# Kernel optimization log

Hardware: AMD Instinct MI355X
Metric: run time of the kernel (lower is better)

## Reference

```python
import jax, jax.numpy as jnp
import numpy as np

BATCH, FIELD_DIM, EMBED_DIM = 16384, 2048, 64


def setup_inputs() -> dict:
    key = jax.random.key(0)
    k1, k2, k3 = jax.random.split(key, 3)
    x = jax.random.normal(k1, (BATCH, FIELD_DIM), dtype=jnp.float32)
    w = jax.random.normal(k2, (FIELD_DIM, 1), dtype=jnp.float32) * 0.02
    b = jnp.zeros((1,), dtype=jnp.float32)
    # FM factor matrix (xavier-normal-ish scale)
    v = jax.random.normal(k3, (FIELD_DIM, EMBED_DIM), dtype=jnp.float32) * (
        (2.0 / (FIELD_DIM + EMBED_DIM)) ** 0.5
    )
    return {"x": x, "w": w, "b": b, "v": v}


def reference(x, w, b, v):
    # First-order linear term: [B, 1]
    linear = x @ w + b
    # Second-order FM term, algebraic reformulation of the O(n^2) pairwise loop:
    # sum_{i<j} <v_i, v_j> x_i x_j = 0.5 * sum_k [(x @ v)_k^2 - (x^2 @ v^2)_k]
    xv = x @ v                       # [B, K]
    x2v2 = (x * x) @ (v * v)         # [B, K]
    second_order = 0.5 * jnp.sum(xv * xv - x2v2, axis=-1, keepdims=True)  # [B, 1]
    return jax.nn.sigmoid(linear + second_order)
```

## Files before the change

kernel.cpp:

```cpp
#include <hip/hip_runtime.h>
#include <stdint.h>

#define FD 2048

typedef short short8 __attribute__((ext_vector_type(8)));
typedef float f32x4 __attribute__((ext_vector_type(4)));
typedef unsigned short ushort_t;

__device__ __forceinline__ unsigned bf16_rne(float f) {
  unsigned u = __float_as_uint(f);
  return (u + 0x7FFFu + ((u >> 16) & 1u)) >> 16;
}

__global__ __launch_bounds__(256) void fm_prep(
    const float* __restrict__ v, ushort_t* __restrict__ hi,
    ushort_t* __restrict__ lo, float* __restrict__ s2t)
{
  int bid = blockIdx.x;
  if (bid < 512) {
    int t = bid * 256 + threadIdx.x;
    int j    = t & 7;
    int lane = (t >> 3) & 63;
    int c    = (t >> 9) & 3;
    int s    = t >> 11;
    int k    = s * 32 + ((lane >> 4) << 3) + j;
    int col  = (c << 4) + (lane & 15);
    float val = v[k * 64 + col];
    unsigned hb = bf16_rne(val);
    float hf = __uint_as_float(hb << 16);
    unsigned lb = bf16_rne(val - hf);
    hi[t] = (ushort_t)hb;
    lo[t] = (ushort_t)lb;
  } else {
    int k = (bid - 512) * 256 + threadIdx.x;
    const float4* row = (const float4*)(v + k * 64);
    float s = 0.f;
    #pragma unroll
    for (int i = 0; i < 16; ++i) {
      float4 q = row[i];
      s += q.x * q.x + q.y * q.y + q.z * q.z + q.w * q.w;
    }
    s2t[k] = s;
  }
}

__global__ __launch_bounds__(512) void fm_main(
    const float* __restrict__ x, const float* __restrict__ w,
    const float* __restrict__ bptr, const short8* __restrict__ vhi,
    const short8* __restrict__ vlo, const float* __restrict__ s2t,
    float* __restrict__ out)
{
  __shared__ float lds_xv[32][64];
  __shared__ float lds_lin[32];
  __shared__ float lds_q[32];

  const int tid = threadIdx.x;
  const int wv  = tid >> 6;
  const int l   = tid & 63;
  const int l15 = l & 15;
  const int lk  = l >> 4;
  const int R   = blockIdx.x << 5;
  const int kbase = wv << 8;

  {
    float* z = &lds_xv[0][0];
    #pragma unroll
    for (int i = tid; i < 32 * 64; i += 512) z[i] = 0.f;
    if (tid < 32) { lds_lin[tid] = 0.f; lds_q[tid] = 0.f; }
  }
  __syncthreads();

  const float* px0 = x + (size_t)(R + l15) * FD + kbase + (lk << 3);
  const float* px1 = px0 + (size_t)16 * FD;
  const float* pw  = w   + kbase + (lk << 3);
  const float* ps  = s2t + kbase + (lk << 3);

  f32x4 acc[2][4];
  #pragma unroll
  for (int t = 0; t < 2; ++t)
    #pragma unroll
    for (int c = 0; c < 4; ++c)
      acc[t][c] = (f32x4){0.f, 0.f, 0.f, 0.f};

  float lin0 = 0.f, lin1 = 0.f, q0 = 0.f, q1 = 0.f;

  #pragma unroll
  for (int st = 0; st < 8; ++st) {
    const int ko = st << 5;
    float4 a0 = *(const float4*)(px0 + ko);
    float4 a1 = *(const float4*)(px0 + ko + 4);
    float4 b0 = *(const float4*)(px1 + ko);
    float4 b1 = *(const float4*)(px1 + ko + 4);
    float4 w0 = *(const float4*)(pw + ko);
    float4 w1 = *(const float4*)(pw + ko + 4);
    float4 s0 = *(const float4*)(ps + ko);
    float4 s1 = *(const float4*)(ps + ko + 4);

    const int sg = (wv << 3) + st;
    short8 bh[4], bl[4];
    #pragma unroll
    for (int c = 0; c < 4; ++c) {
      bh[c] = vhi[(sg * 4 + c) * 64 + l];
      bl[c] = vlo[(sg * 4 + c) * 64 + l];
    }

    float fa[8] = {a0.x, a0.y, a0.z, a0.w, a1.x, a1.y, a1.z, a1.w};
    float fb[8] = {b0.x, b0.y, b0.z, b0.w, b1.x, b1.y, b1.z, b1.w};
    float fw[8] = {w0.x, w0.y, w0.z, w0.w, w1.x, w1.y, w1.z, w1.w};
    float fs[8] = {s0.x, s0.y, s0.z, s0.w, s1.x, s1.y, s1.z, s1.w};

    short8 ah0, al0, ah1, al1;
    #pragma unroll
    for (int j = 0; j < 8; ++j) {
      unsigned h0 = bf16_rne(fa[j]);
      ah0[j] = (short)h0;
      al0[j] = (short)bf16_rne(fa[j] - __uint_as_float(h0 << 16));
      lin0 = fmaf(fa[j], fw[j], lin0);
      q0   = fmaf(fa[j] * fa[j], fs[j], q0);
      unsigned h1 = bf16_rne(fb[j]);
      ah1[j] = (short)h1;
      al1[j] = (short)bf16_rne(fb[j] - __uint_as_float(h1 << 16));
      lin1 = fmaf(fb[j], fw[j], lin1);
      q1   = fmaf(fb[j] * fb[j], fs[j], q1);
    }

    #pragma unroll
    for (int c = 0; c < 4; ++c) {
      acc[0][c] = __builtin_amdgcn_mfma_f32_16x16x32_bf16(ah0, bh[c], acc[0][c], 0, 0, 0);
      acc[0][c] = __builtin_amdgcn_mfma_f32_16x16x32_bf16(al0, bh[c], acc[0][c], 0, 0, 0);
      acc[0][c] = __builtin_amdgcn_mfma_f32_16x16x32_bf16(ah0, bl[c], acc[0][c], 0, 0, 0);
      acc[1][c] = __builtin_amdgcn_mfma_f32_16x16x32_bf16(ah1, bh[c], acc[1][c], 0, 0, 0);
      acc[1][c] = __builtin_amdgcn_mfma_f32_16x16x32_bf16(al1, bh[c], acc[1][c], 0, 0, 0);
      acc[1][c] = __builtin_amdgcn_mfma_f32_16x16x32_bf16(ah1, bl[c], acc[1][c], 0, 0, 0);
    }
  }

  lin0 += __shfl_xor(lin0, 16, 64); lin0 += __shfl_xor(lin0, 32, 64);
  lin1 += __shfl_xor(lin1, 16, 64); lin1 += __shfl_xor(lin1, 32, 64);
  q0   += __shfl_xor(q0,   16, 64); q0   += __shfl_xor(q0,   32, 64);
  q1   += __shfl_xor(q1,   16, 64); q1   += __shfl_xor(q1,   32, 64);
  if (lk == 0) {
    atomicAdd(&lds_lin[l15],      lin0);
    atomicAdd(&lds_lin[16 + l15], lin1);
    atomicAdd(&lds_q[l15],        q0);
    atomicAdd(&lds_q[16 + l15],   q1);
  }

  #pragma unroll
  for (int t = 0; t < 2; ++t)
    #pragma unroll
    for (int c = 0; c < 4; ++c)
      #pragma unroll
      for (int j = 0; j < 4; ++j)
        atomicAdd(&lds_xv[t * 16 + lk * 4 + j][c * 16 + l15], acc[t][c][j]);

  __syncthreads();

  {
    const int row = tid >> 4;
    const int cg  = tid & 15;
    float4 s = *(const float4*)&lds_xv[row][cg << 2];
    float ss = s.x * s.x + s.y * s.y + s.z * s.z + s.w * s.w;
    ss += __shfl_xor(ss, 1, 64);
    ss += __shfl_xor(ss, 2, 64);
    ss += __shfl_xor(ss, 4, 64);
    ss += __shfl_xor(ss, 8, 64);
    if (cg == 0) {
      float z = lds_lin[row] + bptr[0] + 0.5f * (ss - lds_q[row]);
      out[R + row] = 1.f / (1.f + expf(-z));
    }
  }
}

extern "C" void kernel_launch(void* const* d_in, const int* in_sizes, int n_in,
                              void* d_out, int out_size, void* d_ws, size_t ws_size,
                              hipStream_t stream) {
  const float* x = (const float*)d_in[0];
  const float* w = (const float*)d_in[1];
  const float* b = (const float*)d_in[2];
  const float* v = (const float*)d_in[3];
  float* out = (float*)d_out;

  ushort_t* hi = (ushort_t*)d_ws;
  ushort_t* lo = hi + FD * 64;
  float*    s2 = (float*)((char*)d_ws + (size_t)FD * 64 * 2 * sizeof(ushort_t));

  fm_prep<<<520, 256, 0, stream>>>(v, hi, lo, s2);
  fm_main<<<512, 512, 0, stream>>>(x, w, b, (const short8*)hi, (const short8*)lo, s2, out);
}
```

Measured before the change: 256.1 us.

## Software-pipeline x loads and bf16 split conversion, stage w and s2 in LDS

Restructures the main loop so the next step's x tile is loaded and converted to hi/lo bf16 while the current step's MFMAs run, with the MFMAs reordered to group by A operand. The w and s2t vectors are staged once into LDS instead of being reloaded from global memory by every wave. Launch bounds now request 4 blocks per CU. The aim is to hide global-load latency in this memory-bound kernel. The cost is extra register pressure from holding the converted operands across iterations, plus 16 KB more LDS per block.

```diff
diff --git a/kernel.cpp b/kernel.cpp
--- a/kernel.cpp
+++ b/kernel.cpp
@@ -44,12 +44,35 @@
   }
 }
 
-__global__ __launch_bounds__(512) void fm_main(
+__device__ __forceinline__ void cvt_row(
+    const float4& A0, const float4& A1,
+    const float4& W0, const float4& W1,
+    const float4& S0, const float4& S1,
+    short8& H, short8& L, float& lin, float& q)
+{
+  float f[8]  = {A0.x, A0.y, A0.z, A0.w, A1.x, A1.y, A1.z, A1.w};
+  float fw[8] = {W0.x, W0.y, W0.z, W0.w, W1.x, W1.y, W1.z, W1.w};
+  float fs[8] = {S0.x, S0.y, S0.z, S0.w, S1.x, S1.y, S1.z, S1.w};
+  #pragma unroll
+  for (int j = 0; j < 8; ++j) {
+    unsigned h = bf16_rne(f[j]);
+    H[j] = (short)h;
+    L[j] = (short)bf16_rne(f[j] - __uint_as_float(h << 16));
+    lin = fmaf(f[j], fw[j], lin);
+    q   = fmaf(f[j] * f[j], fs[j], q);
+  }
+}
+
+#define MF(accv, a, b) accv = __builtin_amdgcn_mfma_f32_16x16x32_bf16(a, b, accv, 0, 0, 0)
+
+__global__ __launch_bounds__(512, 4) void fm_main(
     const float* __restrict__ x, const float* __restrict__ w,
     const float* __restrict__ bptr, const short8* __restrict__ vhi,
     const short8* __restrict__ vlo, const float* __restrict__ s2t,
     float* __restrict__ out)
 {
+  __shared__ float lds_w[FD];
+  __shared__ float lds_s[FD];
   __shared__ float lds_xv[32][64];
   __shared__ float lds_lin[32];
   __shared__ float lds_q[32];
@@ -67,13 +90,16 @@
     #pragma unroll
     for (int i = tid; i < 32 * 64; i += 512) z[i] = 0.f;
     if (tid < 32) { lds_lin[tid] = 0.f; lds_q[tid] = 0.f; }
+    *(float4*)&lds_w[tid << 2] = *(const float4*)(w + (tid << 2));
+    *(float4*)&lds_s[tid << 2] = *(const float4*)(s2t + (tid << 2));
   }
   __syncthreads();
 
   const float* px0 = x + (size_t)(R + l15) * FD + kbase + (lk << 3);
   const float* px1 = px0 + (size_t)16 * FD;
-  const float* pw  = w   + kbase + (lk << 3);
-  const float* ps  = s2t + kbase + (lk << 3);
+  const int wsoff = kbase + (lk << 3);
+  const short8* pb = vhi + (size_t)wv * 2048 + l;
+  const short8* pl = vlo + (size_t)wv * 2048 + l;
 
   f32x4 acc[2][4];
   #pragma unroll
@@ -84,54 +110,63 @@
 
   float lin0 = 0.f, lin1 = 0.f, q0 = 0.f, q1 = 0.f;
 
+  short8 cah0, cal0, cah1, cal1;
+  {
+    float4 a0 = *(const float4*)(px0);
+    float4 a1 = *(const float4*)(px0 + 4);
+    float4 b0 = *(const float4*)(px1);
+    float4 b1 = *(const float4*)(px1 + 4);
+    float4 wa = *(const float4*)&lds_w[wsoff];
+    float4 wb = *(const float4*)&lds_w[wsoff + 4];
+    float4 sa = *(const float4*)&lds_s[wsoff];
+    float4 sb = *(const float4*)&lds_s[wsoff + 4];
+    cvt_row(a0, a1, wa, wb, sa, sb, cah0, cal0, lin0, q0);
+    cvt_row(b0, b1, wa, wb, sa, sb, cah1, cal1, lin1, q1);
+  }
+
   #pragma unroll
   for (int st = 0; st < 8; ++st) {
-    const int ko = st << 5;
-    float4 a0 = *(const float4*)(px0 + ko);
-    float4 a1 = *(const float4*)(px0 + ko + 4);
-    float4 b0 = *(const float4*)(px1 + ko);
-    float4 b1 = *(const float4*)(px1 + ko + 4);
-    float4 w0 = *(const float4*)(pw + ko);
-    float4 w1 = *(const float4*)(pw + ko + 4);
-    float4 s0 = *(const float4*)(ps + ko);
-    float4 s1 = *(const float4*)(ps + ko + 4);
-
-    const int sg = (wv << 3) + st;
-    short8 bh[4], bl[4];
-    #pragma unroll
-    for (int c = 0; c < 4; ++c) {
-      bh[c] = vhi[(sg * 4 + c) * 64 + l];
-      bl[c] = vlo[(sg * 4 + c) * 64 + l];
-    }
-
-    float fa[8] = {a0.x, a0.y, a0.z, a0.w, a1.x, a1.y, a1.z, a1.w};
-    float fb[8] = {b0.x, b0.y, b0.z, b0.w, b1.x, b1.y, b1.z, b1.w};
-    float fw[8] = {w0.x, w0.y, w0.z, w0.w, w1.x, w1.y, w1.z, w1.w};
-    float fs[8] = {s0.x, s0.y, s0.z, s0.w, s1.x, s1.y, s1.z, s1.w};
-
-    short8 ah0, al0, ah1, al1;
-    #pragma unroll
-    for (int j = 0; j < 8; ++j) {
-      unsigned h0 = bf16_rne(fa[j]);
-      ah0[j] = (short)h0;
-      al0[j] = (short)bf16_rne(fa[j] - __uint_as_float(h0 << 16));
-      lin0 = fmaf(fa[j], fw[j], lin0);
-      q0   = fmaf(fa[j] * fa[j], fs[j], q0);
-      unsigned h1 = bf16_rne(fb[j]);
-      ah1[j] = (short)h1;
-      al1[j] = (short)bf16_rne(fb[j] - __uint_as_float(h1 << 16));
-      lin1 = fmaf(fb[j], fw[j], lin1);
-      q1   = fmaf(fb[j] * fb[j], fs[j], q1);
-    }
-
-    #pragma unroll
-    for (int c = 0; c < 4; ++c) {
-      acc[0][c] = __builtin_amdgcn_mfma_f32_16x16x32_bf16(ah0, bh[c], acc[0][c], 0, 0, 0);
-      acc[0][c] = __builtin_amdgcn_mfma_f32_16x16x32_bf16(al0, bh[c], acc[0][c], 0, 0, 0);
-      acc[0][c] = __builtin_amdgcn_mfma_f32_16x16x32_bf16(ah0, bl[c], acc[0][c], 0, 0, 0);
-      acc[1][c] = __builtin_amdgcn_mfma_f32_16x16x32_bf16(ah1, bh[c], acc[1][c], 0, 0, 0);
-      acc[1][c] = __builtin_amdgcn_mfma_f32_16x16x32_bf16(al1, bh[c], acc[1][c], 0, 0, 0);
-      acc[1][c] = __builtin_amdgcn_mfma_f32_16x16x32_bf16(ah1, bl[c], acc[1][c], 0, 0, 0);
+    float4 na0, na1, nb0, nb1;
+    if (st < 7) {
+      const int nko = (st + 1) << 5;
+      na0 = *(const float4*)(px0 + nko);
+      na1 = *(const float4*)(px0 + nko + 4);
+      nb0 = *(const float4*)(px1 + nko);
+      nb1 = *(const float4*)(px1 + nko + 4);
+    }
+
+    short8 bh0 = pb[st * 256 + 0];
+    short8 bh1 = pb[st * 256 + 64];
+    short8 bh2 = pb[st * 256 + 128];
+    short8 bh3 = pb[st * 256 + 192];
+
+    MF(acc[0][0], cah0, bh0); MF(acc[0][1], cah0, bh1);
+    MF(acc[0][2], cah0, bh2); MF(acc[0][3], cah0, bh3);
+    MF(acc[1][0], cah1, bh0); MF(acc[1][1], cah1, bh1);
+    MF(acc[1][2], cah1, bh2); MF(acc[1][3], cah1, bh3);
+    MF(acc[0][0], cal0, bh0); MF(acc[0][1], cal0, bh1);
+    MF(acc[0][2], cal0, bh2); MF(acc[0][3], cal0, bh3);
+    MF(acc[1][0], cal1, bh0); MF(acc[1][1], cal1, bh1);
+    MF(acc[1][2], cal1, bh2); MF(acc[1][3], cal1, bh3);
+
+    short8 bl0 = pl[st * 256 + 0];
+    short8 bl1 = pl[st * 256 + 64];
+    short8 bl2 = pl[st * 256 + 128];
+    short8 bl3 = pl[st * 256 + 192];
+
+    MF(acc[0][0], cah0, bl0); MF(acc[0][1], cah0, bl1);
+    MF(acc[0][2], cah0, bl2); MF(acc[0][3], cah0, bl3);
+    MF(acc[1][0], cah1, bl0); MF(acc[1][1], cah1, bl1);
+    MF(acc[1][2], cah1, bl2); MF(acc[1][3], cah1, bl3);
+
+    if (st < 7) {
+      const int nws = wsoff + ((st + 1) << 5);
+      float4 wa = *(const float4*)&lds_w[nws];
+      float4 wb = *(const float4*)&lds_w[nws + 4];
+      float4 sa = *(const float4*)&lds_s[nws];
+      float4 sb = *(const float4*)&lds_s[nws + 4];
+      cvt_row(na0, na1, wa, wb, sa, sb, cah0, cal0, lin0, q0);
+      cvt_row(nb0, nb1, wa, wb, sa, sb, cah1, cal1, lin1, q1);
     }
   }
 
```

Measured after the change: 246.0 us. 3.9% less time.

## Stage x tiles into swizzled double-buffered LDS via async global_load_lds

Applied to the files above, without the earlier changes.

Replaces the direct strided per-lane global loads of x with a loop over eight K-tiles. Each tile of 32 rows by 256 columns is copied asynchronously into a double-buffered, XOR-swizzled LDS buffer with global_load_lds, so the next tile's load overlaps the current tile's bf16 split and MFMA work. Work across waves is re-partitioned so all eight waves share each tile instead of each owning a contiguous 256-wide K slice. This adds 64KB of LDS per block plus a barrier per tile, which limits occupancy and adds synchronisation cost.

```diff
diff --git a/kernel.cpp b/kernel.cpp
--- a/kernel.cpp
+++ b/kernel.cpp
@@ -2,10 +2,13 @@
 #include <stdint.h>
 
 #define FD 2048
+#define BK 256
 
 typedef short short8 __attribute__((ext_vector_type(8)));
 typedef float f32x4 __attribute__((ext_vector_type(4)));
 typedef unsigned short ushort_t;
+typedef __attribute__((address_space(3))) char lds_char;
+typedef __attribute__((address_space(1))) const char glb_char;
 
 __device__ __forceinline__ unsigned bf16_rne(float f) {
   unsigned u = __float_as_uint(f);
@@ -44,23 +47,59 @@
   }
 }
 
-__global__ __launch_bounds__(512) void fm_main(
+__device__ __forceinline__ void cvt_row(
+    const f32x4& A0, const f32x4& A1,
+    const f32x4& W0v, const f32x4& W1v,
+    const f32x4& S0, const f32x4& S1,
+    short8& H, short8& L, float& lin, float& q)
+{
+  #pragma unroll
+  for (int j = 0; j < 8; ++j) {
+    float f  = (j < 4) ? A0[j & 3] : A1[j & 3];
+    float fw = (j < 4) ? W0v[j & 3] : W1v[j & 3];
+    float fs = (j < 4) ? S0[j & 3] : S1[j & 3];
+    unsigned h = bf16_rne(f);
+    H[j] = (short)h;
+    L[j] = (short)bf16_rne(f - __uint_as_float(h << 16));
+    lin = fmaf(f, fw, lin);
+    q   = fmaf(f * f, fs, q);
+  }
+}
+
+#define MF(accv, a, b) accv = __builtin_amdgcn_mfma_f32_16x16x32_bf16(a, b, accv, 0, 0, 0)
+
+__global__ __launch_bounds__(512, 4) void fm_main(
     const float* __restrict__ x, const float* __restrict__ w,
     const float* __restrict__ bptr, const short8* __restrict__ vhi,
     const short8* __restrict__ vlo, const float* __restrict__ s2t,
     float* __restrict__ out)
 {
+  __shared__ float xbuf[2][32][BK];
   __shared__ float lds_xv[32][64];
   __shared__ float lds_lin[32];
   __shared__ float lds_q[32];
 
   const int tid = threadIdx.x;
-  const int wv  = tid >> 6;
+  const int wid = tid >> 6;
   const int l   = tid & 63;
   const int l15 = l & 15;
   const int lk  = l >> 4;
+  const int l4  = l << 4;
   const int R   = blockIdx.x << 5;
-  const int kbase = wv << 8;
+
+  #define STAGE(t, b)                                                        \
+    {                                                                        \
+      _Pragma("unroll")                                                      \
+      for (int j = 0; j < 4; ++j) {                                          \
+        const int row = (wid << 2) + j;                                      \
+        const char* src = (const char*)x +                                   \
+            (((size_t)(R + row) << 11) + ((size_t)(t) << 8)) * 4 +           \
+            (size_t)(l4 ^ ((row & 7) << 4));                                 \
+        char* dst = (char*)&xbuf[b][row][0];                                 \
+        __builtin_amdgcn_global_load_lds((glb_char*)src, (lds_char*)dst,     \
+                                         16, 0, 0);                          \
+      }                                                                      \
+    }
 
   {
     float* z = &lds_xv[0][0];
@@ -68,12 +107,8 @@
     for (int i = tid; i < 32 * 64; i += 512) z[i] = 0.f;
     if (tid < 32) { lds_lin[tid] = 0.f; lds_q[tid] = 0.f; }
   }
+  STAGE(0, 0);
   __syncthreads();
-
-  const float* px0 = x + (size_t)(R + l15) * FD + kbase + (lk << 3);
-  const float* px1 = px0 + (size_t)16 * FD;
-  const float* pw  = w   + kbase + (lk << 3);
-  const float* ps  = s2t + kbase + (lk << 3);
 
   f32x4 acc[2][4];
   #pragma unroll
@@ -81,58 +116,58 @@
     #pragma unroll
     for (int c = 0; c < 4; ++c)
       acc[t][c] = (f32x4){0.f, 0.f, 0.f, 0.f};
-
   float lin0 = 0.f, lin1 = 0.f, q0 = 0.f, q1 = 0.f;
 
-  #pragma unroll
-  for (int st = 0; st < 8; ++st) {
-    const int ko = st << 5;
-    float4 a0 = *(const float4*)(px0 + ko);
-    float4 a1 = *(const float4*)(px0 + ko + 4);
-    float4 b0 = *(const float4*)(px1 + ko);
-    float4 b1 = *(const float4*)(px1 + ko + 4);
-    float4 w0 = *(const float4*)(pw + ko);
-    float4 w1 = *(const float4*)(pw + ko + 4);
-    float4 s0 = *(const float4*)(ps + ko);
-    float4 s1 = *(const float4*)(ps + ko + 4);
-
-    const int sg = (wv << 3) + st;
-    short8 bh[4], bl[4];
-    #pragma unroll
-    for (int c = 0; c < 4; ++c) {
-      bh[c] = vhi[(sg * 4 + c) * 64 + l];
-      bl[c] = vlo[(sg * 4 + c) * 64 + l];
-    }
-
-    float fa[8] = {a0.x, a0.y, a0.z, a0.w, a1.x, a1.y, a1.z, a1.w};
-    float fb[8] = {b0.x, b0.y, b0.z, b0.w, b1.x, b1.y, b1.z, b1.w};
-    float fw[8] = {w0.x, w0.y, w0.z, w0.w, w1.x, w1.y, w1.z, w1.w};
-    float fs[8] = {s0.x, s0.y, s0.z, s0.w, s1.x, s1.y, s1.z, s1.w};
-
-    short8 ah0, al0, ah1, al1;
-    #pragma unroll
-    for (int j = 0; j < 8; ++j) {
-      unsigned h0 = bf16_rne(fa[j]);
-      ah0[j] = (short)h0;
-      al0[j] = (short)bf16_rne(fa[j] - __uint_as_float(h0 << 16));
-      lin0 = fmaf(fa[j], fw[j], lin0);
-      q0   = fmaf(fa[j] * fa[j], fs[j], q0);
-      unsigned h1 = bf16_rne(fb[j]);
-      ah1[j] = (short)h1;
-      al1[j] = (short)bf16_rne(fb[j] - __uint_as_float(h1 << 16));
-      lin1 = fmaf(fb[j], fw[j], lin1);
-      q1   = fmaf(fb[j] * fb[j], fs[j], q1);
-    }
-
-    #pragma unroll
-    for (int c = 0; c < 4; ++c) {
-      acc[0][c] = __builtin_amdgcn_mfma_f32_16x16x32_bf16(ah0, bh[c], acc[0][c], 0, 0, 0);
-      acc[0][c] = __builtin_amdgcn_mfma_f32_16x16x32_bf16(al0, bh[c], acc[0][c], 0, 0, 0);
-      acc[0][c] = __builtin_amdgcn_mfma_f32_16x16x32_bf16(ah0, bl[c], acc[0][c], 0, 0, 0);
-      acc[1][c] = __builtin_amdgcn_mfma_f32_16x16x32_bf16(ah1, bh[c], acc[1][c], 0, 0, 0);
-      acc[1][c] = __builtin_amdgcn_mfma_f32_16x16x32_bf16(al1, bh[c], acc[1][c], 0, 0, 0);
-      acc[1][c] = __builtin_amdgcn_mfma_f32_16x16x32_bf16(ah1, bl[c], acc[1][c], 0, 0, 0);
-    }
+  const int sw  = (l15 & 7) << 4;
+  const int cb0 = (wid << 7) + (lk << 5);
+
+  #pragma unroll 1
+  for (int t = 0; t < 8; ++t) {
+    const int b = t & 1;
+
+    const int wo = (t << 8) + (wid << 5) + (lk << 3);
+    f32x4 wa = *(const f32x4*)(w + wo);
+    f32x4 wb = *(const f32x4*)(w + wo + 4);
+    f32x4 sa = *(const f32x4*)(s2t + wo);
+    f32x4 sb = *(const f32x4*)(s2t + wo + 4);
+    const short8* pb = vhi + ((size_t)(((t << 3) + wid) << 2) << 6) / 64 * 64;
+    const short8* plv = vlo + (size_t)(((t << 3) + wid) << 2) * 64;
+    const short8* pbv = vhi + (size_t)(((t << 3) + wid) << 2) * 64;
+    short8 bh0 = pbv[l];        short8 bh1 = pbv[64 + l];
+    short8 bh2 = pbv[128 + l];  short8 bh3 = pbv[192 + l];
+    short8 bl0 = plv[l];        short8 bl1 = plv[64 + l];
+    short8 bl2 = plv[128 + l];  short8 bl3 = plv[192 + l];
+
+    if (t < 7) STAGE(t + 1, b ^ 1);
+
+    {
+      const char* base = (const char*)&xbuf[b][l15][0];
+      f32x4 a0 = *(const f32x4*)(base + (cb0 ^ sw));
+      f32x4 a1 = *(const f32x4*)(base + ((cb0 + 16) ^ sw));
+      short8 cah, cal;
+      cvt_row(a0, a1, wa, wb, sa, sb, cah, cal, lin0, q0);
+      MF(acc[0][0], cah, bh0); MF(acc[0][1], cah, bh1);
+      MF(acc[0][2], cah, bh2); MF(acc[0][3], cah, bh3);
+      MF(acc[0][0], cal, bh0); MF(acc[0][1], cal, bh1);
+      MF(acc[0][2], cal, bh2); MF(acc[0][3], cal, bh3);
+      MF(acc[0][0], cah, bl0); MF(acc[0][1], cah, bl1);
+      MF(acc[0][2], cah, bl2); MF(acc[0][3], cah, bl3);
+    }
+    {
+      const char* base = (const char*)&xbuf[b][l15 + 16][0];
+      f32x4 a0 = *(const f32x4*)(base + (cb0 ^ sw));
+      f32x4 a1 = *(const f32x4*)(base + ((cb0 + 16) ^ sw));
+      short8 cah, cal;
+      cvt_row(a0, a1, wa, wb, sa, sb, cah, cal, lin1, q1);
+      MF(acc[1][0], cah, bh0); MF(acc[1][1], cah, bh1);
+      MF(acc[1][2], cah, bh2); MF(acc[1][3], cah, bh3);
+      MF(acc[1][0], cal, bh0); MF(acc[1][1], cal, bh1);
+      MF(acc[1][2], cal, bh2); MF(acc[1][3], cal, bh3);
+      MF(acc[1][0], cah, bl0); MF(acc[1][1], cah, bl1);
+      MF(acc[1][2], cah, bl2); MF(acc[1][3], cah, bl3);
+    }
+
+    __syncthreads();
   }
 
   lin0 += __shfl_xor(lin0, 16, 64); lin0 += __shfl_xor(lin0, 32, 64);
@@ -152,7 +187,7 @@
     for (int c = 0; c < 4; ++c)
       #pragma unroll
       for (int j = 0; j < 4; ++j)
-        atomicAdd(&lds_xv[t * 16 + lk * 4 + j][c * 16 + l15], acc[t][c][j]);
+        atomicAdd(&lds_xv[t * 16 + (lk << 2) + j][(c << 4) + l15], acc[t][c][j]);
 
   __syncthreads();
 
@@ -166,10 +201,11 @@
     ss += __shfl_xor(ss, 4, 64);
     ss += __shfl_xor(ss, 8, 64);
     if (cg == 0) {
-      float z = lds_lin[row] + bptr[0] + 0.5f * (ss - lds_q[row]);
-      out[R + row] = 1.f / (1.f + expf(-z));
-    }
-  }
+      float zz = lds_lin[row] + bptr[0] + 0.5f * (ss - lds_q[row]);
+      out[R + row] = 1.f / (1.f + expf(-zz));
+    }
+  }
+  #undef STAGE
 }
 
 extern "C" void kernel_launch(void* const* d_in, const int* in_sizes, int n_in,
```

Result: no change. 254.8 us (-0.5%).
